# Kernel optimization log

Hardware: AMD Instinct MI355X
Metric: run time of the kernel (lower is better)

The kernel has to match this reference:

```python
import jax, jax.numpy as jnp
import numpy as np

T, B, I, H, O = 512, 64, 256, 512, 256

def setup_inputs() -> dict:
    key = jax.random.key(0)
    ks = jax.random.split(key, 7)
    s_ih = 1.0 / np.sqrt(H)
    return {
        "x": jax.random.normal(ks[0], (T, B, I), dtype=jnp.float32),
        "W_ih": jax.random.uniform(ks[1], (H, I), jnp.float32, -s_ih, s_ih),
        "W_hh": jax.random.uniform(ks[2], (H, H), jnp.float32, -s_ih, s_ih),
        "b_ih": jax.random.uniform(ks[3], (H,), jnp.float32, -s_ih, s_ih),
        "b_hh": jax.random.uniform(ks[4], (H,), jnp.float32, -s_ih, s_ih),
        "W_out": jax.random.uniform(ks[5], (O, H), jnp.float32, -s_ih, s_ih),
        "b_out": jax.random.uniform(ks[6], (O,), jnp.float32, -s_ih, s_ih),
    }

def reference(x, W_ih, W_hh, b_ih, b_hh, W_out, b_out):
    # Precompute input projection for all timesteps: [T, B, H]
    xp = jnp.einsum('tbi,hi->tbh', x, W_ih) + b_ih + b_hh

    def step(h, xp_t):
        h_new = jnp.tanh(xp_t + h @ W_hh.T)
        return h_new, h_new

    h0 = jnp.zeros((x.shape[1], W_hh.shape[0]), dtype=x.dtype)
    h_last, rnn_out = jax.lax.scan(step, h0, xp)  # rnn_out: [T, B, H]
    y = jnp.einsum('tbh,oh->tbo', rnn_out, W_out) + b_out
    return y, h_last[None]  # h: [1, B, H] matching torch nn.RNN
```

## Files before the change

### kernel.cpp

```cpp
#include <hip/hip_runtime.h>

#define T_DIM 512
#define B_DIM 64
#define I_DIM 256
#define H_DIM 512
#define O_DIM 256

typedef __attribute__((ext_vector_type(8))) short short8;
typedef __attribute__((ext_vector_type(4))) float f32x4;
typedef __attribute__((ext_vector_type(4))) int   i32x4;

__device__ __forceinline__ unsigned short f2bf(float f){
  unsigned int u = __builtin_bit_cast(unsigned int, f);
  u += 0x7fffu + ((u >> 16) & 1u);
  return (unsigned short)(u >> 16);
}
__device__ __forceinline__ float bf2f(unsigned short b){
  unsigned int u = ((unsigned int)b) << 16;
  return __builtin_bit_cast(float, u);
}

#if defined(__has_builtin)
#if __has_builtin(__builtin_amdgcn_update_dpp)
#define HAVE_DPP 1
#endif
#endif

__global__ void pack_bf16(const float* __restrict__ x,
                          const float* __restrict__ wih,
                          const float* __restrict__ wout,
                          unsigned short* __restrict__ xb,
                          unsigned short* __restrict__ wihb,
                          unsigned short* __restrict__ woutb){
  const int NX = (T_DIM*B_DIM*I_DIM)/4;
  const int NW = (H_DIM*I_DIM)/4;
  int i = blockIdx.x * 256 + threadIdx.x;
  const float4* src; unsigned short* dst; int j;
  if (i < NX)          { src = (const float4*)x;    dst = xb;    j = i; }
  else if (i < NX+NW)  { src = (const float4*)wih;  dst = wihb;  j = i - NX; }
  else                 { src = (const float4*)wout; dst = woutb; j = i - NX - NW; }
  float4 f = src[j];
  ushort4 v;
  v.x = f2bf(f.x); v.y = f2bf(f.y); v.z = f2bf(f.z); v.w = f2bf(f.w);
  ((ushort4*)dst)[j] = v;
}

__global__ void quant_whh(const float* __restrict__ W, int* __restrict__ Wq){
  int p = blockIdx.x * blockDim.x + threadIdx.x;
  const float s  = 0.04419417382415922f;
  const float qs = 127.0f / s;
  int out = 0;
  #pragma unroll
  for (int i = 0; i < 4; ++i){
    float w = W[(size_t)p*4 + i];
    int q = __float2int_rn(w * qs);
    q = q < -127 ? -127 : (q > 127 ? 127 : q);
    out |= (q & 0xff) << (8*i);
  }
  Wq[p] = out;
}

__global__
__attribute__((amdgpu_flat_work_group_size(512, 512), amdgpu_waves_per_eu(2, 2)))
void rnn_recur(
    const int* __restrict__ Wq,
    const unsigned short* __restrict__ xp,
    unsigned short* __restrict__ rnn,
    float* __restrict__ hlast)
{
  __shared__ union {
    char H[2][512];
    char occupancy_cap[84 * 1024];
  } sm;
  const int b    = blockIdx.x;
  const int tid  = threadIdx.x;
  const int lane = tid & 63;
  const int wv   = tid >> 6;
  const int lr   = lane & 15;
  const int hi   = lane >> 4;

  const int rloc = 16*((lane >> 2) & 3) + 4*(lane >> 4) + (lane & 3);
  const int row  = 64*wv + rloc;

  i32x4 wf[4][8];
  const char* Wb = (const char*)Wq;
  #pragma unroll
  for (int rt = 0; rt < 4; ++rt){
    const char* rowp = Wb + (size_t)(64*wv + 16*rt + lr)*512 + hi*16;
    #pragma unroll
    for (int kt = 0; kt < 8; ++kt)
      wf[rt][kt] = *(const i32x4*)(rowp + (size_t)kt*64);
  }

  if (tid < 256) ((int*)sm.H)[tid] = 0;

  const float kscale = 0.04419417382415922f / (127.0f * 127.0f);
  const int BH = B_DIM * H_DIM;

  float xp_next = bf2f(xp[(size_t)b*H_DIM + row]);
  float h = 0.0f;
  __syncthreads();

  for (int t = 0; t < T_DIM; ++t){
    float xp_cur = xp_next;
    {
      int tn = (t + 1 < T_DIM) ? (t + 1) : t;
      xp_next = bf2f(xp[(size_t)tn*BH + (size_t)b*H_DIM + row]);
    }

    const char* Hc = sm.H[t & 1];
    i32x4 bf0 = *(const i32x4*)(Hc + 0*64 + hi*16);
    i32x4 bf1 = *(const i32x4*)(Hc + 1*64 + hi*16);
    i32x4 bf2 = *(const i32x4*)(Hc + 2*64 + hi*16);
    i32x4 bf3 = *(const i32x4*)(Hc + 3*64 + hi*16);
    i32x4 bf4 = *(const i32x4*)(Hc + 4*64 + hi*16);
    i32x4 bf5 = *(const i32x4*)(Hc + 5*64 + hi*16);
    i32x4 bf6 = *(const i32x4*)(Hc + 6*64 + hi*16);
    i32x4 bf7 = *(const i32x4*)(Hc + 7*64 + hi*16);

    i32x4 a0 = {0,0,0,0}, a1 = {0,0,0,0}, a2 = {0,0,0,0}, a3 = {0,0,0,0};
    #pragma unroll
    for (int rt = 0; rt < 1; ++rt){}
    a0 = __builtin_amdgcn_mfma_i32_16x16x64_i8(wf[0][0], bf0, a0, 0, 0, 0);
    a1 = __builtin_amdgcn_mfma_i32_16x16x64_i8(wf[1][0], bf0, a1, 0, 0, 0);
    a2 = __builtin_amdgcn_mfma_i32_16x16x64_i8(wf[2][0], bf0, a2, 0, 0, 0);
    a3 = __builtin_amdgcn_mfma_i32_16x16x64_i8(wf[3][0], bf0, a3, 0, 0, 0);
    a0 = __builtin_amdgcn_mfma_i32_16x16x64_i8(wf[0][1], bf1, a0, 0, 0, 0);
    a1 = __builtin_amdgcn_mfma_i32_16x16x64_i8(wf[1][1], bf1, a1, 0, 0, 0);
    a2 = __builtin_amdgcn_mfma_i32_16x16x64_i8(wf[2][1], bf1, a2, 0, 0, 0);
    a3 = __builtin_amdgcn_mfma_i32_16x16x64_i8(wf[3][1], bf1, a3, 0, 0, 0);
    a0 = __builtin_amdgcn_mfma_i32_16x16x64_i8(wf[0][2], bf2, a0, 0, 0, 0);
    a1 = __builtin_amdgcn_mfma_i32_16x16x64_i8(wf[1][2], bf2, a1, 0, 0, 0);
    a2 = __builtin_amdgcn_mfma_i32_16x16x64_i8(wf[2][2], bf2, a2, 0, 0, 0);
    a3 = __builtin_amdgcn_mfma_i32_16x16x64_i8(wf[3][2], bf2, a3, 0, 0, 0);
    a0 = __builtin_amdgcn_mfma_i32_16x16x64_i8(wf[0][3], bf3, a0, 0, 0, 0);
    a1 = __builtin_amdgcn_mfma_i32_16x16x64_i8(wf[1][3], bf3, a1, 0, 0, 0);
    a2 = __builtin_amdgcn_mfma_i32_16x16x64_i8(wf[2][3], bf3, a2, 0, 0, 0);
    a3 = __builtin_amdgcn_mfma_i32_16x16x64_i8(wf[3][3], bf3, a3, 0, 0, 0);
    a0 = __builtin_amdgcn_mfma_i32_16x16x64_i8(wf[0][4], bf4, a0, 0, 0, 0);
    a1 = __builtin_amdgcn_mfma_i32_16x16x64_i8(wf[1][4], bf4, a1, 0, 0, 0);
    a2 = __builtin_amdgcn_mfma_i32_16x16x64_i8(wf[2][4], bf4, a2, 0, 0, 0);
    a3 = __builtin_amdgcn_mfma_i32_16x16x64_i8(wf[3][4], bf4, a3, 0, 0, 0);
    a0 = __builtin_amdgcn_mfma_i32_16x16x64_i8(wf[0][5], bf5, a0, 0, 0, 0);
    a1 = __builtin_amdgcn_mfma_i32_16x16x64_i8(wf[1][5], bf5, a1, 0, 0, 0);
    a2 = __builtin_amdgcn_mfma_i32_16x16x64_i8(wf[2][5], bf5, a2, 0, 0, 0);
    a3 = __builtin_amdgcn_mfma_i32_16x16x64_i8(wf[3][5], bf5, a3, 0, 0, 0);
    a0 = __builtin_amdgcn_mfma_i32_16x16x64_i8(wf[0][6], bf6, a0, 0, 0, 0);
    a1 = __builtin_amdgcn_mfma_i32_16x16x64_i8(wf[1][6], bf6, a1, 0, 0, 0);
    a2 = __builtin_amdgcn_mfma_i32_16x16x64_i8(wf[2][6], bf6, a2, 0, 0, 0);
    a3 = __builtin_amdgcn_mfma_i32_16x16x64_i8(wf[3][6], bf6, a3, 0, 0, 0);
    a0 = __builtin_amdgcn_mfma_i32_16x16x64_i8(wf[0][7], bf7, a0, 0, 0, 0);
    a1 = __builtin_amdgcn_mfma_i32_16x16x64_i8(wf[1][7], bf7, a1, 0, 0, 0);
    a2 = __builtin_amdgcn_mfma_i32_16x16x64_i8(wf[2][7], bf7, a2, 0, 0, 0);
    a3 = __builtin_amdgcn_mfma_i32_16x16x64_i8(wf[3][7], bf7, a3, 0, 0, 0);

    int f0, f1, f2, f3;
    {
      int e0 = (lane & 4) ? a1[0] : a0[0];
      int e1 = (lane & 4) ? a3[0] : a2[0];
      f0 = (lane & 8) ? e1 : e0;
      e0 = (lane & 4) ? a1[1] : a0[1];
      e1 = (lane & 4) ? a3[1] : a2[1];
      f1 = (lane & 8) ? e1 : e0;
      e0 = (lane & 4) ? a1[2] : a0[2];
      e1 = (lane & 4) ? a3[2] : a2[2];
      f2 = (lane & 8) ? e1 : e0;
      e0 = (lane & 4) ? a1[3] : a0[3];
      e1 = (lane & 4) ? a3[3] : a2[3];
      f3 = (lane & 8) ? e1 : e0;
    }
    int g0 = (lane & 1) ? f1 : f0;
    int g1 = (lane & 1) ? f3 : f2;
    int am = (lane & 2) ? g1 : g0;

    float pre = xp_cur + (float)am * kscale;
    float aa = fabsf(pre);
    float e  = __expf(-2.0f * aa);
    float r  = (1.0f - e) * __builtin_amdgcn_rcpf(1.0f + e);
    h = copysignf(r, pre);

    rnn[(size_t)t*BH + (size_t)b*H_DIM + row] = f2bf(h);

    int q = __float2int_rn(h * 127.0f) & 0xff;
#ifdef HAVE_DPP
    int p1 = __builtin_amdgcn_update_dpp(0, q, 0xB1, 0xf, 0xf, true);
    int y  = q | (p1 << 8);
    int p2 = __builtin_amdgcn_update_dpp(0, y, 0x4E, 0xf, 0xf, true);
    int z  = y | (p2 << 16);
    if ((lane & 3) == 0) ((int*)sm.H[(t + 1) & 1])[row >> 2] = z;
#else
    sm.H[(t + 1) & 1][row] = (char)q;
#endif
    asm volatile("s_waitcnt lgkmcnt(0)" ::: "memory");
    __builtin_amdgcn_s_barrier();
  }
  hlast[(size_t)b*H_DIM + row] = h;
}

template<typename TA, typename TB, typename TO>
__global__ __launch_bounds__(256) void gemm_bt(
    const TA* __restrict__ A, const TB* __restrict__ B, TO* __restrict__ C,
    const float* __restrict__ bias1, const float* __restrict__ bias2,
    int M, int N, int K)
{
  __shared__ unsigned short As[64][40];
  __shared__ unsigned short Bs[64][40];
  const int tid  = threadIdx.x;
  const int m0   = blockIdx.y * 64;
  const int n0   = blockIdx.x * 64;
  const int srow = tid >> 2, skc = tid & 3;
  const int lane = tid & 63, wid = tid >> 6;
  const int wm   = wid >> 1, wn = wid & 1;
  const int lr   = lane & 15, lq = lane >> 4;

  f32x4 acc[2][2];
  #pragma unroll
  for (int i = 0; i < 2; ++i)
    #pragma unroll
    for (int j = 0; j < 2; ++j) acc[i][j] = (f32x4){0.f, 0.f, 0.f, 0.f};

  for (int k0 = 0; k0 < K; k0 += 32){
    {
      const TA* src = A + (size_t)(m0 + srow)*K + k0 + skc*8;
      uint4 v;
      if constexpr (__is_same(TA, float)){
        float4 f0 = *(const float4*)src;
        float4 f1 = *(const float4*)(src + 4);
        v.x = (unsigned)f2bf(f0.x) | ((unsigned)f2bf(f0.y) << 16);
        v.y = (unsigned)f2bf(f0.z) | ((unsigned)f2bf(f0.w) << 16);
        v.z = (unsigned)f2bf(f1.x) | ((unsigned)f2bf(f1.y) << 16);
        v.w = (unsigned)f2bf(f1.z) | ((unsigned)f2bf(f1.w) << 16);
      } else {
        v = *(const uint4*)src;
      }
      *(uint4*)&As[srow][skc*8] = v;
    }
    {
      const TB* src = B + (size_t)(n0 + srow)*K + k0 + skc*8;
      uint4 v;
      if constexpr (__is_same(TB, float)){
        float4 f0 = *(const float4*)src;
        float4 f1 = *(const float4*)(src + 4);
        v.x = (unsigned)f2bf(f0.x) | ((unsigned)f2bf(f0.y) << 16);
        v.y = (unsigned)f2bf(f0.z) | ((unsigned)f2bf(f0.w) << 16);
        v.z = (unsigned)f2bf(f1.x) | ((unsigned)f2bf(f1.y) << 16);
        v.w = (unsigned)f2bf(f1.z) | ((unsigned)f2bf(f1.w) << 16);
      } else {
        v = *(const uint4*)src;
      }
      *(uint4*)&Bs[srow][skc*8] = v;
    }
    __syncthreads();
    uint4 av0 = *(const uint4*)&As[wm*32      + lr][lq*8];
    uint4 av1 = *(const uint4*)&As[wm*32 + 16 + lr][lq*8];
    uint4 bv0 = *(const uint4*)&Bs[wn*32      + lr][lq*8];
    uint4 bv1 = *(const uint4*)&Bs[wn*32 + 16 + lr][lq*8];
    short8 a0 = __builtin_bit_cast(short8, av0);
    short8 a1 = __builtin_bit_cast(short8, av1);
    short8 b0 = __builtin_bit_cast(short8, bv0);
    short8 b1 = __builtin_bit_cast(short8, bv1);
    acc[0][0] = __builtin_amdgcn_mfma_f32_16x16x32_bf16(a0, b0, acc[0][0], 0, 0, 0);
    acc[0][1] = __builtin_amdgcn_mfma_f32_16x16x32_bf16(a0, b1, acc[0][1], 0, 0, 0);
    acc[1][0] = __builtin_amdgcn_mfma_f32_16x16x32_bf16(a1, b0, acc[1][0], 0, 0, 0);
    acc[1][1] = __builtin_amdgcn_mfma_f32_16x16x32_bf16(a1, b1, acc[1][1], 0, 0, 0);
    __syncthreads();
  }

  #pragma unroll
  for (int i = 0; i < 2; ++i)
    #pragma unroll
    for (int j = 0; j < 2; ++j)
      #pragma unroll
      for (int r = 0; r < 4; ++r){
        int grow = m0 + wm*32 + i*16 + lq*4 + r;
        int gcol = n0 + wn*32 + j*16 + lr;
        float v = acc[i][j][r] + bias1[gcol];
        if (bias2) v += bias2[gcol];
        if constexpr (__is_same(TO, float)) C[(size_t)grow*N + gcol] = v;
        else                                C[(size_t)grow*N + gcol] = f2bf(v);
      }
}

extern "C" void kernel_launch(void* const* d_in, const int* in_sizes, int n_in,
                              void* d_out, int out_size, void* d_ws, size_t ws_size,
                              hipStream_t stream){
  (void)in_sizes; (void)n_in; (void)out_size; (void)ws_size;
  const float* x    = (const float*)d_in[0];
  const float* Wih  = (const float*)d_in[1];
  const float* Whh  = (const float*)d_in[2];
  const float* bih  = (const float*)d_in[3];
  const float* bhh  = (const float*)d_in[4];
  const float* Wout = (const float*)d_in[5];
  const float* bout = (const float*)d_in[6];
  float* y     = (float*)d_out;
  float* hlast = y + (size_t)T_DIM * B_DIM * O_DIM;

  char* ws = (char*)d_ws;
  const size_t MB = 1024*1024;
  unsigned short* xp   = (unsigned short*)ws;
  unsigned short* rnn  = (unsigned short*)(ws + 32*MB);
  unsigned short* xb   = (unsigned short*)(ws + 32*MB);
  unsigned short* wihb = (unsigned short*)(ws + 48*MB);
  int*            Wq   = (int*)           (ws + 64*MB);
  unsigned short* wob  = (unsigned short*)(ws + 64*MB + 256*1024);

  pack_bf16<<<8448, 256, 0, stream>>>(x, Wih, Wout, xb, wihb, wob);
  quant_whh<<<256, 256, 0, stream>>>(Whh, Wq);
  gemm_bt<unsigned short, unsigned short, unsigned short><<<dim3(8, 512), 256, 0, stream>>>(
      xb, wihb, xp, bih, bhh, T_DIM*B_DIM, H_DIM, I_DIM);
  rnn_recur<<<64, 512, 0, stream>>>(Wq, xp, rnn, hlast);
  gemm_bt<unsigned short, unsigned short, float><<<dim3(4, 512), 256, 0, stream>>>(
      rnn, wob, y, bout, nullptr, T_DIM*B_DIM, O_DIM, H_DIM);
}
```

Measured before the change: 498.2 us.

## Merge pack kernels, simplify tanh, and use 128x128 GEMM tiles

Folds the W_hh int8 quantization into the bf16 packing kernel, which removes one launch. Rewrites tanh in the recurrence as 1-2/(exp(2x)+1), with the factor of 2 folded into the xp value and the scale. This drops the fabs and copysign steps from the serial critical path. Enlarges the GEMM tiles from 64x64 to 128x128 with a 4x4 MFMA accumulator per wave, for more data reuse per LDS load, at the cost of more registers and fewer blocks. The new tanh form can hit exp overflow for large inputs, but the reciprocal of infinity still yields -1/1 correctly.

After: 499.2 us. No clear change (+0.2%).

```diff
diff --git a/kernel.cpp b/kernel.cpp
--- a/kernel.cpp
+++ b/kernel.cpp
@@ -26,38 +26,40 @@
 #endif
 #endif
 
-__global__ void pack_bf16(const float* __restrict__ x,
-                          const float* __restrict__ wih,
-                          const float* __restrict__ wout,
-                          unsigned short* __restrict__ xb,
-                          unsigned short* __restrict__ wihb,
-                          unsigned short* __restrict__ woutb){
+__global__ void pack_all(const float* __restrict__ x,
+                         const float* __restrict__ wih,
+                         const float* __restrict__ wout,
+                         const float* __restrict__ whh,
+                         unsigned short* __restrict__ xb,
+                         unsigned short* __restrict__ wihb,
+                         unsigned short* __restrict__ woutb,
+                         int* __restrict__ Wq){
   const int NX = (T_DIM*B_DIM*I_DIM)/4;
   const int NW = (H_DIM*I_DIM)/4;
   int i = blockIdx.x * 256 + threadIdx.x;
-  const float4* src; unsigned short* dst; int j;
-  if (i < NX)          { src = (const float4*)x;    dst = xb;    j = i; }
-  else if (i < NX+NW)  { src = (const float4*)wih;  dst = wihb;  j = i - NX; }
-  else                 { src = (const float4*)wout; dst = woutb; j = i - NX - NW; }
-  float4 f = src[j];
-  ushort4 v;
-  v.x = f2bf(f.x); v.y = f2bf(f.y); v.z = f2bf(f.z); v.w = f2bf(f.w);
-  ((ushort4*)dst)[j] = v;
-}
-
-__global__ void quant_whh(const float* __restrict__ W, int* __restrict__ Wq){
-  int p = blockIdx.x * blockDim.x + threadIdx.x;
-  const float s  = 0.04419417382415922f;
-  const float qs = 127.0f / s;
-  int out = 0;
-  #pragma unroll
-  for (int i = 0; i < 4; ++i){
-    float w = W[(size_t)p*4 + i];
-    int q = __float2int_rn(w * qs);
-    q = q < -127 ? -127 : (q > 127 ? 127 : q);
-    out |= (q & 0xff) << (8*i);
-  }
-  Wq[p] = out;
+  if (i < NX + 2*NW){
+    const float4* src; unsigned short* dst; int j;
+    if (i < NX)          { src = (const float4*)x;    dst = xb;    j = i; }
+    else if (i < NX+NW)  { src = (const float4*)wih;  dst = wihb;  j = i - NX; }
+    else                 { src = (const float4*)wout; dst = woutb; j = i - NX - NW; }
+    float4 f = src[j];
+    ushort4 v;
+    v.x = f2bf(f.x); v.y = f2bf(f.y); v.z = f2bf(f.z); v.w = f2bf(f.w);
+    ((ushort4*)dst)[j] = v;
+  } else {
+    int p = i - (NX + 2*NW);
+    const float s  = 0.04419417382415922f;
+    const float qs = 127.0f / s;
+    int out = 0;
+    #pragma unroll
+    for (int k = 0; k < 4; ++k){
+      float w = whh[(size_t)p*4 + k];
+      int q = __float2int_rn(w * qs);
+      q = q < -127 ? -127 : (q > 127 ? 127 : q);
+      out |= (q & 0xff) << (8*k);
+    }
+    Wq[p] = out;
+  }
 }
 
 __global__
@@ -94,18 +96,18 @@
 
   if (tid < 256) ((int*)sm.H)[tid] = 0;
 
-  const float kscale = 0.04419417382415922f / (127.0f * 127.0f);
+  const float kscale2 = 2.0f * 0.04419417382415922f / (127.0f * 127.0f);
   const int BH = B_DIM * H_DIM;
 
-  float xp_next = bf2f(xp[(size_t)b*H_DIM + row]);
+  float xp2_next = 2.0f * bf2f(xp[(size_t)b*H_DIM + row]);
   float h = 0.0f;
   __syncthreads();
 
   for (int t = 0; t < T_DIM; ++t){
-    float xp_cur = xp_next;
+    float xp2_cur = xp2_next;
     {
       int tn = (t + 1 < T_DIM) ? (t + 1) : t;
-      xp_next = bf2f(xp[(size_t)tn*BH + (size_t)b*H_DIM + row]);
+      xp2_next = 2.0f * bf2f(xp[(size_t)tn*BH + (size_t)b*H_DIM + row]);
     }
 
     const char* Hc = sm.H[t & 1];
@@ -119,8 +121,6 @@
     i32x4 bf7 = *(const i32x4*)(Hc + 7*64 + hi*16);
 
     i32x4 a0 = {0,0,0,0}, a1 = {0,0,0,0}, a2 = {0,0,0,0}, a3 = {0,0,0,0};
-    #pragma unroll
-    for (int rt = 0; rt < 1; ++rt){}
     a0 = __builtin_amdgcn_mfma_i32_16x16x64_i8(wf[0][0], bf0, a0, 0, 0, 0);
     a1 = __builtin_amdgcn_mfma_i32_16x16x64_i8(wf[1][0], bf0, a1, 0, 0, 0);
     a2 = __builtin_amdgcn_mfma_i32_16x16x64_i8(wf[2][0], bf0, a2, 0, 0, 0);
@@ -173,11 +173,10 @@
     int g1 = (lane & 1) ? f3 : f2;
     int am = (lane & 2) ? g1 : g0;
 
-    float pre = xp_cur + (float)am * kscale;
-    float aa = fabsf(pre);
-    float e  = __expf(-2.0f * aa);
-    float r  = (1.0f - e) * __builtin_amdgcn_rcpf(1.0f + e);
-    h = copysignf(r, pre);
+    float pre2 = xp2_cur + (float)am * kscale2;
+    float e2 = __expf(pre2);
+    float rc = __builtin_amdgcn_rcpf(e2 + 1.0f);
+    h = fmaf(-2.0f, rc, 1.0f);
 
     rnn[(size_t)t*BH + (size_t)b*H_DIM + row] = f2bf(h);
 
@@ -197,83 +196,58 @@
   hlast[(size_t)b*H_DIM + row] = h;
 }
 
-template<typename TA, typename TB, typename TO>
-__global__ __launch_bounds__(256) void gemm_bt(
-    const TA* __restrict__ A, const TB* __restrict__ B, TO* __restrict__ C,
+template<typename TO>
+__global__ __launch_bounds__(256) void gemm_bt128(
+    const unsigned short* __restrict__ A, const unsigned short* __restrict__ B,
+    TO* __restrict__ C,
     const float* __restrict__ bias1, const float* __restrict__ bias2,
     int M, int N, int K)
 {
-  __shared__ unsigned short As[64][40];
-  __shared__ unsigned short Bs[64][40];
+  __shared__ unsigned short As[128][40];
+  __shared__ unsigned short Bs[128][40];
   const int tid  = threadIdx.x;
-  const int m0   = blockIdx.y * 64;
-  const int n0   = blockIdx.x * 64;
-  const int srow = tid >> 2, skc = tid & 3;
   const int lane = tid & 63, wid = tid >> 6;
+  const int m0   = blockIdx.y * 128;
+  const int n0   = blockIdx.x * 128;
   const int wm   = wid >> 1, wn = wid & 1;
   const int lr   = lane & 15, lq = lane >> 4;
-
-  f32x4 acc[2][2];
+  const int sr0  = tid >> 2, so = tid & 3;
+  const int sr1  = 64 + sr0;
+
+  f32x4 acc[4][4];
   #pragma unroll
-  for (int i = 0; i < 2; ++i)
-    #pragma unroll
-    for (int j = 0; j < 2; ++j) acc[i][j] = (f32x4){0.f, 0.f, 0.f, 0.f};
+  for (int i = 0; i < 4; ++i)
+    #pragma unroll
+    for (int j = 0; j < 4; ++j) acc[i][j] = (f32x4){0.f, 0.f, 0.f, 0.f};
 
   for (int k0 = 0; k0 < K; k0 += 32){
-    {
-      const TA* src = A + (size_t)(m0 + srow)*K + k0 + skc*8;
-      uint4 v;
-      if constexpr (__is_same(TA, float)){
-        float4 f0 = *(const float4*)src;
-        float4 f1 = *(const float4*)(src + 4);
-        v.x = (unsigned)f2bf(f0.x) | ((unsigned)f2bf(f0.y) << 16);
-        v.y = (unsigned)f2bf(f0.z) | ((unsigned)f2bf(f0.w) << 16);
-        v.z = (unsigned)f2bf(f1.x) | ((unsigned)f2bf(f1.y) << 16);
-        v.w = (unsigned)f2bf(f1.z) | ((unsigned)f2bf(f1.w) << 16);
-      } else {
-        v = *(const uint4*)src;
-      }
-      *(uint4*)&As[srow][skc*8] = v;
-    }
-    {
-      const TB* src = B + (size_t)(n0 + srow)*K + k0 + skc*8;
-      uint4 v;
-      if constexpr (__is_same(TB, float)){
-        float4 f0 = *(const float4*)src;
-        float4 f1 = *(const float4*)(src + 4);
-        v.x = (unsigned)f2bf(f0.x) | ((unsigned)f2bf(f0.y) << 16);
-        v.y = (unsigned)f2bf(f0.z) | ((unsigned)f2bf(f0.w) << 16);
-        v.z = (unsigned)f2bf(f1.x) | ((unsigned)f2bf(f1.y) << 16);
-        v.w = (unsigned)f2bf(f1.z) | ((unsigned)f2bf(f1.w) << 16);
-      } else {
-        v = *(const uint4*)src;
-      }
-      *(uint4*)&Bs[srow][skc*8] = v;
-    }
+    *(uint4*)&As[sr0][so*8] = *(const uint4*)(A + (size_t)(m0 + sr0)*K + k0 + so*8);
+    *(uint4*)&As[sr1][so*8] = *(const uint4*)(A + (size_t)(m0 + sr1)*K + k0 + so*8);
+    *(uint4*)&Bs[sr0][so*8] = *(const uint4*)(B + (size_t)(n0 + sr0)*K + k0 + so*8);
+    *(uint4*)&Bs[sr1][so*8] = *(const uint4*)(B + (size_t)(n0 + sr1)*K + k0 + so*8);
     __syncthreads();
-    uint4 av0 = *(const uint4*)&As[wm*32      + lr][lq*8];
-    uint4 av1 = *(const uint4*)&As[wm*32 + 16 + lr][lq*8];
-    uint4 bv0 = *(const uint4*)&Bs[wn*32      + lr][lq*8];
-    uint4 bv1 = *(const uint4*)&Bs[wn*32 + 16 + lr][lq*8];
-    short8 a0 = __builtin_bit_cast(short8, av0);
-    short8 a1 = __builtin_bit_cast(short8, av1);
-    short8 b0 = __builtin_bit_cast(short8, bv0);
-    short8 b1 = __builtin_bit_cast(short8, bv1);
-    acc[0][0] = __builtin_amdgcn_mfma_f32_16x16x32_bf16(a0, b0, acc[0][0], 0, 0, 0);
-    acc[0][1] = __builtin_amdgcn_mfma_f32_16x16x32_bf16(a0, b1, acc[0][1], 0, 0, 0);
-    acc[1][0] = __builtin_amdgcn_mfma_f32_16x16x32_bf16(a1, b0, acc[1][0], 0, 0, 0);
-    acc[1][1] = __builtin_amdgcn_mfma_f32_16x16x32_bf16(a1, b1, acc[1][1], 0, 0, 0);
+    short8 a[4], bfr[4];
+    #pragma unroll
+    for (int i = 0; i < 4; ++i){
+      a[i]   = __builtin_bit_cast(short8, *(const uint4*)&As[wm*64 + i*16 + lr][lq*8]);
+      bfr[i] = __builtin_bit_cast(short8, *(const uint4*)&Bs[wn*64 + i*16 + lr][lq*8]);
+    }
+    #pragma unroll
+    for (int i = 0; i < 4; ++i)
+      #pragma unroll
+      for (int j = 0; j < 4; ++j)
+        acc[i][j] = __builtin_amdgcn_mfma_f32_16x16x32_bf16(a[i], bfr[j], acc[i][j], 0, 0, 0);
     __syncthreads();
   }
 
   #pragma unroll
-  for (int i = 0; i < 2; ++i)
-    #pragma unroll
-    for (int j = 0; j < 2; ++j)
+  for (int i = 0; i < 4; ++i)
+    #pragma unroll
+    for (int j = 0; j < 4; ++j)
       #pragma unroll
       for (int r = 0; r < 4; ++r){
-        int grow = m0 + wm*32 + i*16 + lq*4 + r;
-        int gcol = n0 + wn*32 + j*16 + lr;
+        int grow = m0 + wm*64 + i*16 + lq*4 + r;
+        int gcol = n0 + wn*64 + j*16 + lr;
         float v = acc[i][j][r] + bias1[gcol];
         if (bias2) v += bias2[gcol];
         if constexpr (__is_same(TO, float)) C[(size_t)grow*N + gcol] = v;
@@ -304,11 +278,10 @@
   int*            Wq   = (int*)           (ws + 64*MB);
   unsigned short* wob  = (unsigned short*)(ws + 64*MB + 256*1024);
 
-  pack_bf16<<<8448, 256, 0, stream>>>(x, Wih, Wout, xb, wihb, wob);
-  quant_whh<<<256, 256, 0, stream>>>(Whh, Wq);
-  gemm_bt<unsigned short, unsigned short, unsigned short><<<dim3(8, 512), 256, 0, stream>>>(
+  pack_all<<<8704, 256, 0, stream>>>(x, Wih, Wout, Whh, xb, wihb, wob, Wq);
+  gemm_bt128<unsigned short><<<dim3(4, 256), 256, 0, stream>>>(
       xb, wihb, xp, bih, bhh, T_DIM*B_DIM, H_DIM, I_DIM);
   rnn_recur<<<64, 512, 0, stream>>>(Wq, xp, rnn, hlast);
-  gemm_bt<unsigned short, unsigned short, float><<<dim3(4, 512), 256, 0, stream>>>(
+  gemm_bt128<float><<<dim3(2, 256), 256, 0, stream>>>(
       rnn, wob, y, bout, nullptr, T_DIM*B_DIM, O_DIM, H_DIM);
 }
```
